# Kernel optimization log

Hardware: AMD Instinct MI355X
Metric: run time of the kernel (lower is better)

Reference implementation:

```python
import jax, jax.numpy as jnp
import numpy as np

B, CI, H, W = 16, 32, 224, 224
CO, K, STRIDE = 32, 3, 1


def setup_inputs() -> dict:
    key = jax.random.key(0)
    k1, k2, k3 = jax.random.split(key, 3)
    x = jax.random.normal(k1, (B, CI, H, W), dtype=jnp.float32)
    weights = jax.random.normal(k2, (CO, CI, K, K), dtype=jnp.float32)
    bias = jax.random.normal(k3, (CO,), dtype=jnp.float32)
    return {"x": x, "weights": weights, "bias": bias}


def reference(x, weights, bias):
    # Faithful to HandmadeConv2D with padding=0, stride=1: a VALID
    # cross-correlation (the torch code never actually pads x) plus bias.
    out = jax.lax.conv_general_dilated(
        x, weights,
        window_strides=(STRIDE, STRIDE),
        padding="VALID",
        dimension_numbers=("NCHW", "OIHW", "NCHW"),
    )
    return out + bias[None, :, None, None]
```

## Files before the change

### kernel.cpp

```cpp
#include <hip/hip_runtime.h>
#include <hip/hip_bf16.h>

#define B_  16
#define CI_ 32
#define H_  224
#define W_  224
#define CO_ 32
#define OH_ 222
#define OW_ 222
#define HW_ (H_*W_)
#define K_  288
#define ROWSTR (W_*CI_)

#define XT_OFF   32768
#define XT_BYTES ((size_t)B_ * HW_ * CI_ * 2)

typedef __attribute__((ext_vector_type(8))) short short8;
typedef __attribute__((ext_vector_type(4))) float float4v;
typedef float float4u __attribute__((ext_vector_type(4), aligned(4)));

__global__ void wprep(const float* __restrict__ w, unsigned short* __restrict__ wbf) {
    int idx = blockIdx.x * 256 + threadIdx.x;
    if (idx >= CO_ * K_) return;
    int co  = idx / K_;
    int rem = idx - co * K_;
    int ci  = rem / 9;
    int g   = rem - ci * 9;
    unsigned int u = __float_as_uint(w[idx]);
    u = u + 0x7FFFu + ((u >> 16) & 1u);
    wbf[co * K_ + g * 32 + ci] = (unsigned short)(u >> 16);
}

__global__ __launch_bounds__(256) void xform(const float* __restrict__ x,
                                             unsigned short* __restrict__ xT) {
    const int pix = blockIdx.x * 256 + threadIdx.x;
    const int b   = blockIdx.y;
    const float* xp = x + (size_t)b * CI_ * HW_ + pix;
    unsigned short* op = xT + ((size_t)b * HW_ + pix) * CI_;
    float f[CI_];
#pragma unroll
    for (int ci = 0; ci < CI_; ++ci) f[ci] = xp[(size_t)ci * HW_];
    union { short8 s8[4]; __hip_bfloat162 h2[16]; } u;
#pragma unroll
    for (int i = 0; i < 16; ++i)
        u.h2[i] = __float22bfloat162_rn(make_float2(f[2*i], f[2*i+1]));
#pragma unroll
    for (int i = 0; i < 4; ++i)
        *(short8*)&op[i * 8] = u.s8[i];
}

__global__ __launch_bounds__(256) void conv_mfma(
    const unsigned short* __restrict__ xT, const unsigned short* __restrict__ wbf,
    const float* __restrict__ bias, float* __restrict__ out)
{
    const int t    = threadIdx.x;
    const int lane = t & 63;
    const int wv   = t >> 6;
    const int i16  = lane & 15;
    const int quad = lane >> 4;
    const int ow0  = blockIdx.x * 64;
    const int oh   = blockIdx.y * 4 + wv;
    const int b    = blockIdx.z;
    if (oh >= OH_) return;

    int aoff[4];
#pragma unroll
    for (int ot = 0; ot < 4; ++ot) {
        int px = ow0 + ot * 16 + i16;
        if (px > OW_ - 1) px = OW_ - 1;
        aoff[ot] = px * CI_ + quad * 8;
    }
    const unsigned short* xb  = xT + (size_t)b * HW_ * CI_;
    const unsigned short* wr0 = wbf + (size_t)i16 * K_;
    const unsigned short* wr1 = wbf + (size_t)(16 + i16) * K_;

    float4v acc[4][2] = {};

#pragma unroll
    for (int g = 0; g < 9; ++g) {
        const int kh = g / 3;
        const int kw = g - kh * 3;
        const short8 b0 = *(const short8*)&wr0[g * 32 + quad * 8];
        const short8 b1 = *(const short8*)&wr1[g * 32 + quad * 8];
        const unsigned short* rbase = xb + (size_t)(oh + kh) * ROWSTR + kw * CI_;
#pragma unroll
        for (int ot = 0; ot < 4; ++ot) {
            const short8 a = *(const short8*)&rbase[aoff[ot]];
            acc[ot][0] = __builtin_amdgcn_mfma_f32_16x16x32_bf16(a, b0, acc[ot][0], 0, 0, 0);
            acc[ot][1] = __builtin_amdgcn_mfma_f32_16x16x32_bf16(a, b1, acc[ot][1], 0, 0, 0);
        }
    }

    const float bv0 = bias[i16];
    const float bv1 = bias[16 + i16];
    const size_t o0 = ((size_t)(b * CO_ + i16) * OH_ + oh) * (size_t)OW_;
    const size_t o1 = ((size_t)(b * CO_ + 16 + i16) * OH_ + oh) * (size_t)OW_;
#pragma unroll
    for (int ot = 0; ot < 4; ++ot) {
        const int owq = ow0 + ot * 16 + quad * 4;
        float4u v0 = { acc[ot][0][0] + bv0, acc[ot][0][1] + bv0,
                       acc[ot][0][2] + bv0, acc[ot][0][3] + bv0 };
        float4u v1 = { acc[ot][1][0] + bv1, acc[ot][1][1] + bv1,
                       acc[ot][1][2] + bv1, acc[ot][1][3] + bv1 };
        if (owq + 3 < OW_) {
            *(float4u*)&out[o0 + owq] = v0;
            *(float4u*)&out[o1 + owq] = v1;
        } else {
#pragma unroll
            for (int r = 0; r < 4; ++r) {
                if (owq + r < OW_) {
                    out[o0 + owq + r] = acc[ot][0][r] + bv0;
                    out[o1 + owq + r] = acc[ot][1][r] + bv1;
                }
            }
        }
    }
}

#define XCOLS 66
#define CISTR 40
__global__ __launch_bounds__(256) void conv_fb(
    const float* __restrict__ x, const unsigned short* __restrict__ wbf,
    const float* __restrict__ bias, float* __restrict__ out)
{
    __shared__ unsigned short Xs[3 * XCOLS * CISTR];
    const int t    = threadIdx.x;
    const int lane = t & 63;
    const int wv   = t >> 6;
    const int ow0  = blockIdx.x * 64;
    const int oh   = blockIdx.y;
    const int b    = blockIdx.z;
    {
        const int col = t & 63;
        const int ci0 = (t >> 6) * 8;
        const float* xb = x + (size_t)b * CI_ * HW_;
#pragma unroll
        for (int kh = 0; kh < 3; ++kh) {
            const float* base = xb + (size_t)(oh + kh) * W_ + ow0;
            for (int rep = 0; rep < 2; ++rep) {
                const int c2 = rep == 0 ? col : 64 + col;
                if (rep == 1 && col >= 2) break;
                const bool v = (ow0 + c2) < W_;
                float f[8];
#pragma unroll
                for (int i = 0; i < 8; ++i)
                    f[i] = v ? base[(size_t)(ci0 + i) * HW_ + c2] : 0.0f;
                union { short8 s8; __hip_bfloat162 h2[4]; } u;
#pragma unroll
                for (int i = 0; i < 4; ++i)
                    u.h2[i] = __float22bfloat162_rn(make_float2(f[2*i], f[2*i+1]));
                *(short8*)&Xs[(kh * XCOLS + c2) * CISTR + ci0] = u.s8;
            }
        }
    }
    __syncthreads();
    const int i16  = lane & 15;
    const int quad = lane >> 4;
    float4v acc0 = {0.f,0.f,0.f,0.f}, acc1 = {0.f,0.f,0.f,0.f};
    const unsigned short* wr0 = wbf + (size_t)i16 * K_;
    const unsigned short* wr1 = wbf + (size_t)(16 + i16) * K_;
#pragma unroll
    for (int g = 0; g < 9; ++g) {
        const int kh = g / 3, kw = g - kh * 3;
        const short8 a  = *(const short8*)&Xs[(kh * XCOLS + wv * 16 + i16 + kw) * CISTR + quad * 8];
        const short8 b0 = *(const short8*)&wr0[g * 32 + quad * 8];
        const short8 b1 = *(const short8*)&wr1[g * 32 + quad * 8];
        acc0 = __builtin_amdgcn_mfma_f32_16x16x32_bf16(a, b0, acc0, 0, 0, 0);
        acc1 = __builtin_amdgcn_mfma_f32_16x16x32_bf16(a, b1, acc1, 0, 0, 0);
    }
    const float bv0 = bias[i16], bv1 = bias[16 + i16];
    const int owbase = ow0 + wv * 16 + quad * 4;
    const size_t o0 = ((size_t)(b * CO_ + i16) * OH_ + oh) * (size_t)OW_;
    const size_t o1 = ((size_t)(b * CO_ + 16 + i16) * OH_ + oh) * (size_t)OW_;
#pragma unroll
    for (int r = 0; r < 4; ++r) {
        const int ow = owbase + r;
        if (ow < OW_) { out[o0 + ow] = acc0[r] + bv0; out[o1 + ow] = acc1[r] + bv1; }
    }
}

extern "C" void kernel_launch(void* const* d_in, const int* in_sizes, int n_in,
                              void* d_out, int out_size, void* d_ws, size_t ws_size,
                              hipStream_t stream) {
    const float* x    = (const float*)d_in[0];
    const float* w    = (const float*)d_in[1];
    const float* bias = (const float*)d_in[2];
    float* out        = (float*)d_out;
    unsigned short* wbf = (unsigned short*)d_ws;

    wprep<<<(CO_ * K_ + 255) / 256, 256, 0, stream>>>(w, wbf);

    if (ws_size >= XT_OFF + XT_BYTES) {
        unsigned short* xT = (unsigned short*)((char*)d_ws + XT_OFF);
        xform<<<dim3(HW_ / 256, B_), 256, 0, stream>>>(x, xT);
        dim3 grid((OW_ + 63) / 64, (OH_ + 3) / 4, B_);
        conv_mfma<<<grid, 256, 0, stream>>>(xT, wbf, bias, out);
    } else {
        dim3 grid((OW_ + 63) / 64, OH_, B_);
        conv_fb<<<grid, 256, 0, stream>>>(x, wbf, bias, out);
    }
}
```

Baseline: 272.5 us.

## Fuse NCHW-to-bf16 transform into conv kernel via shared-memory halo tiles

Measured after the change: 224.8 us. 1.21x faster.

```diff
diff --git a/kernel.cpp b/kernel.cpp
--- a/kernel.cpp
+++ b/kernel.cpp
@@ -10,10 +10,15 @@
 #define OW_ 222
 #define HW_ (H_*W_)
 #define K_  288
-#define ROWSTR (W_*CI_)
 
-#define XT_OFF   32768
-#define XT_BYTES ((size_t)B_ * HW_ * CI_ * 2)
+#define OHB   8
+#define ROWS  10
+#define OWT   64
+#define PXT   66
+#define NOHB  28
+#define NOWT  4
+#define NTASK (ROWS*PXT)
+#define NBLK  (NOHB*NOWT*B_)
 
 typedef __attribute__((ext_vector_type(8))) short short8;
 typedef __attribute__((ext_vector_type(4))) float float4v;
@@ -31,46 +36,51 @@
     wbf[co * K_ + g * 32 + ci] = (unsigned short)(u >> 16);
 }
 
-__global__ __launch_bounds__(256) void xform(const float* __restrict__ x,
-                                             unsigned short* __restrict__ xT) {
-    const int pix = blockIdx.x * 256 + threadIdx.x;
-    const int b   = blockIdx.y;
-    const float* xp = x + (size_t)b * CI_ * HW_ + pix;
-    unsigned short* op = xT + ((size_t)b * HW_ + pix) * CI_;
-    float f[CI_];
-#pragma unroll
-    for (int ci = 0; ci < CI_; ++ci) f[ci] = xp[(size_t)ci * HW_];
-    union { short8 s8[4]; __hip_bfloat162 h2[16]; } u;
-#pragma unroll
-    for (int i = 0; i < 16; ++i)
-        u.h2[i] = __float22bfloat162_rn(make_float2(f[2*i], f[2*i+1]));
-#pragma unroll
-    for (int i = 0; i < 4; ++i)
-        *(short8*)&op[i * 8] = u.s8[i];
-}
-
-__global__ __launch_bounds__(256) void conv_mfma(
-    const unsigned short* __restrict__ xT, const unsigned short* __restrict__ wbf,
+__global__ __launch_bounds__(512, 4) void conv_fused(
+    const float* __restrict__ x, const unsigned short* __restrict__ wbf,
     const float* __restrict__ bias, float* __restrict__ out)
 {
-    const int t    = threadIdx.x;
+    __shared__ unsigned short Xs[NTASK * CI_];
+
+    const int t   = threadIdx.x;
+    const int bid = blockIdx.x;
+    const int xcd   = bid & 7;
+    const int owt   = (bid >> 3) & 3;
+    const int gid   = (bid >> 5) * 8 + xcd;
+    const int b     = gid / NOHB;
+    const int ohblk = gid - b * NOHB;
+    const int r0    = ohblk * OHB;
+    const int ow0   = owt * OWT;
+
+    for (int task = t; task < NTASK; task += 512) {
+        const int tr = task / PXT;
+        const int p  = task - tr * PXT;
+        int row = r0 + tr;  if (row > H_ - 1) row = H_ - 1;
+        int col = ow0 + p;  if (col > W_ - 1) col = W_ - 1;
+        const float* xp = x + (size_t)b * CI_ * HW_ + (size_t)row * W_ + col;
+        unsigned short* dst = &Xs[task * CI_];
+#pragma unroll
+        for (int h = 0; h < 2; ++h) {
+            float f[16];
+#pragma unroll
+            for (int j = 0; j < 16; ++j) f[j] = xp[(size_t)(h * 16 + j) * HW_];
+            union { short8 s8[2]; __hip_bfloat162 h2[8]; } u;
+#pragma unroll
+            for (int i = 0; i < 8; ++i)
+                u.h2[i] = __float22bfloat162_rn(make_float2(f[2*i], f[2*i+1]));
+            *(short8*)&dst[h * 16]     = u.s8[0];
+            *(short8*)&dst[h * 16 + 8] = u.s8[1];
+        }
+    }
+    __syncthreads();
+
     const int lane = t & 63;
     const int wv   = t >> 6;
+    const int oh   = r0 + wv;
+    if (oh >= OH_) return;
     const int i16  = lane & 15;
     const int quad = lane >> 4;
-    const int ow0  = blockIdx.x * 64;
-    const int oh   = blockIdx.y * 4 + wv;
-    const int b    = blockIdx.z;
-    if (oh >= OH_) return;
 
-    int aoff[4];
-#pragma unroll
-    for (int ot = 0; ot < 4; ++ot) {
-        int px = ow0 + ot * 16 + i16;
-        if (px > OW_ - 1) px = OW_ - 1;
-        aoff[ot] = px * CI_ + quad * 8;
-    }
-    const unsigned short* xb  = xT + (size_t)b * HW_ * CI_;
     const unsigned short* wr0 = wbf + (size_t)i16 * K_;
     const unsigned short* wr1 = wbf + (size_t)(16 + i16) * K_;
 
@@ -82,10 +92,11 @@
         const int kw = g - kh * 3;
         const short8 b0 = *(const short8*)&wr0[g * 32 + quad * 8];
         const short8 b1 = *(const short8*)&wr1[g * 32 + quad * 8];
-        const unsigned short* rbase = xb + (size_t)(oh + kh) * ROWSTR + kw * CI_;
+        const unsigned short* ar =
+            &Xs[((wv + kh) * PXT + i16 + kw) * CI_ + quad * 8];
 #pragma unroll
         for (int ot = 0; ot < 4; ++ot) {
-            const short8 a = *(const short8*)&rbase[aoff[ot]];
+            const short8 a = *(const short8*)&ar[ot * 16 * CI_];
             acc[ot][0] = __builtin_amdgcn_mfma_f32_16x16x32_bf16(a, b0, acc[ot][0], 0, 0, 0);
             acc[ot][1] = __builtin_amdgcn_mfma_f32_16x16x32_bf16(a, b1, acc[ot][1], 0, 0, 0);
         }
@@ -117,68 +128,6 @@
     }
 }
 
-#define XCOLS 66
-#define CISTR 40
-__global__ __launch_bounds__(256) void conv_fb(
-    const float* __restrict__ x, const unsigned short* __restrict__ wbf,
-    const float* __restrict__ bias, float* __restrict__ out)
-{
-    __shared__ unsigned short Xs[3 * XCOLS * CISTR];
-    const int t    = threadIdx.x;
-    const int lane = t & 63;
-    const int wv   = t >> 6;
-    const int ow0  = blockIdx.x * 64;
-    const int oh   = blockIdx.y;
-    const int b    = blockIdx.z;
-    {
-        const int col = t & 63;
-        const int ci0 = (t >> 6) * 8;
-        const float* xb = x + (size_t)b * CI_ * HW_;
-#pragma unroll
-        for (int kh = 0; kh < 3; ++kh) {
-            const float* base = xb + (size_t)(oh + kh) * W_ + ow0;
-            for (int rep = 0; rep < 2; ++rep) {
-                const int c2 = rep == 0 ? col : 64 + col;
-                if (rep == 1 && col >= 2) break;
-                const bool v = (ow0 + c2) < W_;
-                float f[8];
-#pragma unroll
-                for (int i = 0; i < 8; ++i)
-                    f[i] = v ? base[(size_t)(ci0 + i) * HW_ + c2] : 0.0f;
-                union { short8 s8; __hip_bfloat162 h2[4]; } u;
-#pragma unroll
-                for (int i = 0; i < 4; ++i)
-                    u.h2[i] = __float22bfloat162_rn(make_float2(f[2*i], f[2*i+1]));
-                *(short8*)&Xs[(kh * XCOLS + c2) * CISTR + ci0] = u.s8;
-            }
-        }
-    }
-    __syncthreads();
-    const int i16  = lane & 15;
-    const int quad = lane >> 4;
-    float4v acc0 = {0.f,0.f,0.f,0.f}, acc1 = {0.f,0.f,0.f,0.f};
-    const unsigned short* wr0 = wbf + (size_t)i16 * K_;
-    const unsigned short* wr1 = wbf + (size_t)(16 + i16) * K_;
-#pragma unroll
-    for (int g = 0; g < 9; ++g) {
-        const int kh = g / 3, kw = g - kh * 3;
-        const short8 a  = *(const short8*)&Xs[(kh * XCOLS + wv * 16 + i16 + kw) * CISTR + quad * 8];
-        const short8 b0 = *(const short8*)&wr0[g * 32 + quad * 8];
-        const short8 b1 = *(const short8*)&wr1[g * 32 + quad * 8];
-        acc0 = __builtin_amdgcn_mfma_f32_16x16x32_bf16(a, b0, acc0, 0, 0, 0);
-        acc1 = __builtin_amdgcn_mfma_f32_16x16x32_bf16(a, b1, acc1, 0, 0, 0);
-    }
-    const float bv0 = bias[i16], bv1 = bias[16 + i16];
-    const int owbase = ow0 + wv * 16 + quad * 4;
-    const size_t o0 = ((size_t)(b * CO_ + i16) * OH_ + oh) * (size_t)OW_;
-    const size_t o1 = ((size_t)(b * CO_ + 16 + i16) * OH_ + oh) * (size_t)OW_;
-#pragma unroll
-    for (int r = 0; r < 4; ++r) {
-        const int ow = owbase + r;
-        if (ow < OW_) { out[o0 + ow] = acc0[r] + bv0; out[o1 + ow] = acc1[r] + bv1; }
-    }
-}
-
 extern "C" void kernel_launch(void* const* d_in, const int* in_sizes, int n_in,
                               void* d_out, int out_size, void* d_ws, size_t ws_size,
                               hipStream_t stream) {
@@ -189,14 +138,5 @@
     unsigned short* wbf = (unsigned short*)d_ws;
 
     wprep<<<(CO_ * K_ + 255) / 256, 256, 0, stream>>>(w, wbf);
-
-    if (ws_size >= XT_OFF + XT_BYTES) {
-        unsigned short* xT = (unsigned short*)((char*)d_ws + XT_OFF);
-        xform<<<dim3(HW_ / 256, B_), 256, 0, stream>>>(x, xT);
-        dim3 grid((OW_ + 63) / 64, (OH_ + 3) / 4, B_);
-        conv_mfma<<<grid, 256, 0, stream>>>(xT, wbf, bias, out);
-    } else {
-        dim3 grid((OW_ + 63) / 64, OH_, B_);
-        conv_fb<<<grid, 256, 0, stream>>>(x, wbf, bias, out);
-    }
+    conv_fused<<<dim3(NBLK), 512, 0, stream>>>(x, wbf, bias, out);
 }
```
